# Kernel tuning notes

Measured on AMD Instinct MI355X. Metric: run time of the kernel, lower is better.

The kernel has to match this reference:

```python
import jax, jax.numpy as jnp
import numpy as np

# Dimensions: N batch, C chromosomes, GPC genes per chromosome, H hidden, S signature
N, C, GPC, H, S = 4096, 25, 80, 8, 32
G = C * GPC  # total genes (= input feature count D)
NB_CAT = 3   # each gene column is categorical in {0,1,2}
BN_EPS = 1e-5


def setup_inputs() -> dict:
    key = jax.random.key(0)
    k0, k1, k2, k3, k4 = jax.random.split(key, 5)
    # categorical gene columns
    x = jax.random.randint(k0, (N, G), 0, NB_CAT)
    # one embedding table per gene (genes_emb_sharing=False): (G, 3, H)
    emb_tables = jax.random.normal(k1, (G, NB_CAT, H), dtype=jnp.float32)
    # block-structured chromosome composition matrix (C, G): contiguous gene ranges
    cm = np.zeros((C, G), dtype=np.float32)
    for c in range(C):
        cm[c, c * GPC:(c + 1) * GPC] = 1.0
    chrom_mask = jnp.asarray(cm)
    # attention parameters (init: standard normal, as in the torch module)
    gene_att = jax.random.normal(k2, (C, H), dtype=jnp.float32)
    chrom_att = jax.random.normal(k3, (H,), dtype=jnp.float32)
    # final linear layer H -> S
    W = jax.random.normal(k4, (H, S), dtype=jnp.float32) / np.sqrt(H).astype(np.float32)
    b = jnp.zeros((S,), dtype=jnp.float32)
    return {"x": x, "emb_tables": emb_tables, "chrom_mask": chrom_mask,
            "gene_att": gene_att, "chrom_att": chrom_att, "W": W, "b": b}


def reference(x, emb_tables, chrom_mask, gene_att, chrom_att, W, b):
    G_ = emb_tables.shape[0]
    # entity embedding: per-gene table lookup -> (N, G, H)
    h = emb_tables[jnp.arange(G_)[None, :], x]

    # --- GeneAttentionLayer ---
    # fused form of einsum('ij,njk->nijk') -> transpose -> einsum('ij,kijm->kim'):
    # att[n,c,g] = chrom_mask[c,g] * <gene_att[c], h[n,g]>   (N, C, G)
    att = jnp.einsum('ch,ngh->ncg', gene_att, h) * chrom_mask[None]
    m = jax.lax.stop_gradient((att != 0).astype(att.dtype))  # detached byte mask
    att = jnp.exp(jax.nn.leaky_relu(att)) * m                # slope 0.01 matches torch
    att = att / att.sum(axis=2, keepdims=True)               # group softmax over genes
    chrom_emb = jnp.einsum('ncg,ngh->nch', att, h)           # (N, C, H)
    chrom_emb = jax.nn.relu(chrom_emb)

    # --- ChromAttentionLayer ---
    a = jnp.einsum('h,nch->nc', chrom_att, chrom_emb)        # (N, C)
    a = jnp.exp(jax.nn.leaky_relu(a))
    a = a / a.sum(axis=1, keepdims=True)
    sig = jnp.einsum('nc,nch->nh', a, chrom_emb)             # (N, H)
    sig = jax.nn.relu(sig)

    # linear + BatchNorm1d (training mode, gamma=1, beta=0, biased var)
    out = sig @ W + b
    mu = out.mean(axis=0)
    var = out.var(axis=0)
    return (out - mu) / jnp.sqrt(var + BN_EPS)
```

## Files before the change

### kernel.cpp

```cpp
#include <hip/hip_runtime.h>
#include <hip/hip_bf16.h>

#define NN   4096
#define CC   25
#define GPCg 80
#define HH   8
#define SS   32
#define GG   2000
#define TROWS 6000
#define SMB  16
#define NBLK (NN/SMB)
#define NQ   128
#define NTASK (SMB*CC)

#define CSTRIDE 241
#define A16_BYTES  96512
#define ATT_BYTES  12064
#define CE_BYTES   12800
#define SMEM_BYTES (A16_BYTES + ATT_BYTES + CE_BYTES)

typedef _Float16 h8 __attribute__((ext_vector_type(8)));

#define WS_RAW  0
#define WS_PART 131072

template<int CTRL>
__device__ __forceinline__ float dpp_add(float x) {
    int y = __builtin_amdgcn_mov_dpp(__float_as_int(x), CTRL, 0xF, 0xF, true);
    return x + __int_as_float(y);
}
__device__ __forceinline__ float red4(float x) {
    x = dpp_add<0xB1>(x);
    x = dpp_add<0x4E>(x);
    return x;
}

__global__ __launch_bounds__(512, 1) void k_fused(
    const int*   __restrict__ x, const float* __restrict__ emb,
    const float* __restrict__ gene_att, const float* __restrict__ chrom_att,
    const float* __restrict__ W, const float* __restrict__ b,
    float* __restrict__ raw, float2* __restrict__ part)
{
    extern __shared__ __align__(16) char smem[];
    _Float16* A16s  = (_Float16*)smem;
    _Float16* Att16 = (_Float16*)(smem + A16_BYTES);
    float*    ce    = (float*)(smem + A16_BYTES + ATT_BYTES);

    const int bid = blockIdx.x;
    const int n0  = bid * SMB;
    const int tid = threadIdx.x;
    const int qid = tid >> 2;
    const int q   = tid & 3;

    auto prefetch = [&](int r, int* dst) {
        const int task = r * NQ + qid;
        if (task < NTASK) {
            const int sm = task / CC;
            const int c  = task - sm * CC;
            const int* xp = x + (size_t)(n0 + sm) * GG + c * GPCg + q;
            #pragma unroll
            for (int j = 0; j < 20; ++j) dst[j] = xp[4 * j];
        }
    };

    auto compute = [&](int r, const int* xv) {
        const int task = r * NQ + qid;
        if (task < NTASK) {
            const int sm = task / CC;
            const int c  = task - sm * CC;
            const int base = c * CSTRIDE + 3 * q;

            h8 acc0, acc1;
            #pragma unroll
            for (int h = 0; h < HH; ++h) { acc0[h] = (_Float16)0.f; acc1[h] = (_Float16)0.f; }
            float asum = 0.f;

            #pragma unroll
            for (int j = 0; j < 20; ++j) {
                const int p = base + j * 12 + xv[j];
                h8 a = *(const h8*)(A16s + (size_t)p * HH);
                if (j & 1) acc1 += a; else acc0 += a;
                asum += (float)Att16[p];
            }

            float f0 = (float)acc0[0] + (float)acc1[0];
            float f1 = (float)acc0[1] + (float)acc1[1];
            float f2 = (float)acc0[2] + (float)acc1[2];
            float f3 = (float)acc0[3] + (float)acc1[3];
            float f4 = (float)acc0[4] + (float)acc1[4];
            float f5 = (float)acc0[5] + (float)acc1[5];
            float f6 = (float)acc0[6] + (float)acc1[6];
            float f7 = (float)acc0[7] + (float)acc1[7];
            f0 = red4(f0); f1 = red4(f1); f2 = red4(f2); f3 = red4(f3);
            f4 = red4(f4); f5 = red4(f5); f6 = red4(f6); f7 = red4(f7);
            asum = red4(asum);

            const float s = 1.f / asum;
            float va = f0, vb = f1;
            if (q == 1) { va = f2; vb = f3; }
            if (q == 2) { va = f4; vb = f5; }
            if (q == 3) { va = f6; vb = f7; }
            va = fmaxf(va * s, 0.f);
            vb = fmaxf(vb * s, 0.f);
            *(float2*)(ce + sm * (CC*HH) + c * HH + 2 * q) = make_float2(va, vb);
        }
    };

    int bufA[20], bufB[20];

    prefetch(0, bufA);

    for (int l = tid; l < TROWS; l += 512) {
        const int g    = l / 3;
        const int xv   = l - g * 3;
        const int c    = g / GPCg;
        const int gloc = g - c * GPCg;
        const int p    = c * CSTRIDE + gloc * 3 + xv;

        const float4* ep = (const float4*)(emb + (size_t)l * HH);
        float4 e0 = ep[0], e1 = ep[1];
        float ev[HH] = {e0.x, e0.y, e0.z, e0.w, e1.x, e1.y, e1.z, e1.w};
        float logit = 0.f;
        #pragma unroll
        for (int h = 0; h < HH; ++h) logit += gene_att[c * HH + h] * ev[h];
        float att = 0.f;
        if (logit != 0.f) {
            float lr = (logit >= 0.f) ? logit : 0.01f * logit;
            att = expf(lr);
        }
        h8 rr;
        #pragma unroll
        for (int h = 0; h < HH; ++h) rr[h] = (_Float16)(att * ev[h] * 0.00390625f);
        *(h8*)(A16s + (size_t)p * HH) = rr;
        Att16[p] = (_Float16)(att * 0.00390625f);
    }
    __syncthreads();

    prefetch(1, bufB); compute(0, bufA);
    prefetch(2, bufA); compute(1, bufB);
    prefetch(3, bufB); compute(2, bufA);
    compute(3, bufB);
    __syncthreads();

    const int half = tid >> 5;
    const int j    = tid & 31;
    const int n    = n0 + half;

    float cev[HH];
    float a = 0.f;
    if (j < CC) {
        const float4* p4 = (const float4*)(ce + half * (CC*HH) + j * HH);
        float4 v0 = p4[0], v1 = p4[1];
        cev[0]=v0.x; cev[1]=v0.y; cev[2]=v0.z; cev[3]=v0.w;
        cev[4]=v1.x; cev[5]=v1.y; cev[6]=v1.z; cev[7]=v1.w;
        float d = 0.f;
        #pragma unroll
        for (int h = 0; h < HH; ++h) d += chrom_att[h] * cev[h];
        float lr = (d >= 0.f) ? d : 0.01f * d;
        a = expf(lr);
    } else {
        #pragma unroll
        for (int h = 0; h < HH; ++h) cev[h] = 0.f;
    }

    float asum2 = a;
    #pragma unroll
    for (int off = 16; off >= 1; off >>= 1) asum2 += __shfl_xor(asum2, off, 32);
    const float an = a / asum2;

    float sig[HH];
    #pragma unroll
    for (int h = 0; h < HH; ++h) sig[h] = an * cev[h];
    #pragma unroll
    for (int off = 16; off >= 1; off >>= 1) {
        #pragma unroll
        for (int h = 0; h < HH; ++h) sig[h] += __shfl_xor(sig[h], off, 32);
    }
    #pragma unroll
    for (int h = 0; h < HH; ++h) sig[h] = fmaxf(sig[h], 0.f);

    float o = b[j];
    #pragma unroll
    for (int h = 0; h < HH; ++h) o += sig[h] * W[h * SS + j];
    raw[(size_t)n * SS + j] = o;

    float* psum = (float*)smem;
    float* psq  = psum + SMB * SS;
    psum[half * SS + j] = o;
    psq [half * SS + j] = o * o;
    __syncthreads();
    if (tid < SS) {
        float s1 = 0.f, s2 = 0.f;
        #pragma unroll
        for (int r = 0; r < SMB; ++r) { s1 += psum[r * SS + tid]; s2 += psq[r * SS + tid]; }
        part[(size_t)bid * SS + tid] = make_float2(s1, s2);
    }
}

__global__ __launch_bounds__(256) void k_bn(
    const float2* __restrict__ part, const float* __restrict__ raw,
    float* __restrict__ out)
{
    __shared__ float a1[8][SS], a2[8][SS];
    __shared__ float2 ms[SS];

    const int tid   = threadIdx.x;
    const int col   = tid & 31;
    const int chunk = tid >> 5;

    float s1 = 0.f, s2 = 0.f;
    for (int i = chunk * 32; i < chunk * 32 + 32; ++i) {
        float2 p = part[(size_t)i * SS + col];
        s1 += p.x; s2 += p.y;
    }
    a1[chunk][col] = s1; a2[chunk][col] = s2;
    __syncthreads();
    if (tid < SS) {
        float t1 = 0.f, t2 = 0.f;
        #pragma unroll
        for (int r = 0; r < 8; ++r) { t1 += a1[r][tid]; t2 += a2[r][tid]; }
        float mu  = t1 / (float)NN;
        float var = t2 / (float)NN - mu * mu;
        ms[tid] = make_float2(mu, rsqrtf(var + 1e-5f));
    }
    __syncthreads();

    const int n_loc = tid >> 3;
    const int s4    = tid & 7;
    const size_t off = ((size_t)(blockIdx.x * 32 + n_loc) * SS) + s4 * 4;
    float4 v = *(const float4*)(raw + off);
    float4 o;
    o.x = (v.x - ms[s4*4+0].x) * ms[s4*4+0].y;
    o.y = (v.y - ms[s4*4+1].x) * ms[s4*4+1].y;
    o.z = (v.z - ms[s4*4+2].x) * ms[s4*4+2].y;
    o.w = (v.w - ms[s4*4+3].x) * ms[s4*4+3].y;
    *(float4*)(out + off) = o;
}

extern "C" void kernel_launch(void* const* d_in, const int* in_sizes, int n_in,
                              void* d_out, int out_size, void* d_ws, size_t ws_size,
                              hipStream_t stream) {
    const int*   x         = (const int*)  d_in[0];
    const float* emb       = (const float*)d_in[1];
    const float* gene_att  = (const float*)d_in[3];
    const float* chrom_att = (const float*)d_in[4];
    const float* W         = (const float*)d_in[5];
    const float* b         = (const float*)d_in[6];
    float* out = (float*)d_out;

    float*  fws  = (float*)d_ws;
    float*  raw  = fws + WS_RAW;
    float2* part = (float2*)(fws + WS_PART);

    (void)hipFuncSetAttribute((const void*)k_fused,
                              hipFuncAttributeMaxDynamicSharedMemorySize,
                              (int)SMEM_BYTES);

    k_fused<<<NBLK, 512, SMEM_BYTES, stream>>>(x, emb, gene_att, chrom_att, W, b, raw, part);
    k_bn   <<<NN/32, 256, 0, stream>>>(part, raw, out);
}
```

Baseline: 22.01 us.

## Use 1024-thread blocks with two lanes per task and upfront x loads

The fused kernel now launches 1024 threads per block. Each (sample, chromosome) task is handled by a pair of lanes covering 40 genes each, instead of four lanes over four software-pipelined rounds. All categorical indices are loaded into registers before the table-build phase, so the global loads overlap with the shared-memory table construction and no longer need prefetch rounds. This costs more registers per thread (40 indices) and a larger block, leaving 400 of the 512 lane pairs doing work.

Measured after the change: 33.16 us. +50.6%, slower.

```diff
diff --git a/kernel.cpp b/kernel.cpp
--- a/kernel.cpp
+++ b/kernel.cpp
@@ -10,7 +10,8 @@
 #define TROWS 6000
 #define SMB  16
 #define NBLK (NN/SMB)
-#define NQ   128
+#define NTH  1024
+#define NPAIR (NTH/2)
 #define NTASK (SMB*CC)
 
 #define CSTRIDE 241
@@ -29,13 +30,11 @@
     int y = __builtin_amdgcn_mov_dpp(__float_as_int(x), CTRL, 0xF, 0xF, true);
     return x + __int_as_float(y);
 }
-__device__ __forceinline__ float red4(float x) {
-    x = dpp_add<0xB1>(x);
-    x = dpp_add<0x4E>(x);
-    return x;
-}
-
-__global__ __launch_bounds__(512, 1) void k_fused(
+__device__ __forceinline__ float red2(float x) {
+    return dpp_add<0xB1>(x);
+}
+
+__global__ __launch_bounds__(NTH, 1) void k_fused(
     const int*   __restrict__ x, const float* __restrict__ emb,
     const float* __restrict__ gene_att, const float* __restrict__ chrom_att,
     const float* __restrict__ W, const float* __restrict__ b,
@@ -49,80 +48,33 @@
     const int bid = blockIdx.x;
     const int n0  = bid * SMB;
     const int tid = threadIdx.x;
-    const int qid = tid >> 2;
-    const int q   = tid & 3;
-
-    auto prefetch = [&](int r, int* dst) {
-        const int task = r * NQ + qid;
-        if (task < NTASK) {
-            const int sm = task / CC;
-            const int c  = task - sm * CC;
-            const int* xp = x + (size_t)(n0 + sm) * GG + c * GPCg + q;
-            #pragma unroll
-            for (int j = 0; j < 20; ++j) dst[j] = xp[4 * j];
-        }
-    };
-
-    auto compute = [&](int r, const int* xv) {
-        const int task = r * NQ + qid;
-        if (task < NTASK) {
-            const int sm = task / CC;
-            const int c  = task - sm * CC;
-            const int base = c * CSTRIDE + 3 * q;
-
-            h8 acc0, acc1;
-            #pragma unroll
-            for (int h = 0; h < HH; ++h) { acc0[h] = (_Float16)0.f; acc1[h] = (_Float16)0.f; }
-            float asum = 0.f;
-
-            #pragma unroll
-            for (int j = 0; j < 20; ++j) {
-                const int p = base + j * 12 + xv[j];
-                h8 a = *(const h8*)(A16s + (size_t)p * HH);
-                if (j & 1) acc1 += a; else acc0 += a;
-                asum += (float)Att16[p];
-            }
-
-            float f0 = (float)acc0[0] + (float)acc1[0];
-            float f1 = (float)acc0[1] + (float)acc1[1];
-            float f2 = (float)acc0[2] + (float)acc1[2];
-            float f3 = (float)acc0[3] + (float)acc1[3];
-            float f4 = (float)acc0[4] + (float)acc1[4];
-            float f5 = (float)acc0[5] + (float)acc1[5];
-            float f6 = (float)acc0[6] + (float)acc1[6];
-            float f7 = (float)acc0[7] + (float)acc1[7];
-            f0 = red4(f0); f1 = red4(f1); f2 = red4(f2); f3 = red4(f3);
-            f4 = red4(f4); f5 = red4(f5); f6 = red4(f6); f7 = red4(f7);
-            asum = red4(asum);
-
-            const float s = 1.f / asum;
-            float va = f0, vb = f1;
-            if (q == 1) { va = f2; vb = f3; }
-            if (q == 2) { va = f4; vb = f5; }
-            if (q == 3) { va = f6; vb = f7; }
-            va = fmaxf(va * s, 0.f);
-            vb = fmaxf(vb * s, 0.f);
-            *(float2*)(ce + sm * (CC*HH) + c * HH + 2 * q) = make_float2(va, vb);
-        }
-    };
-
-    int bufA[20], bufB[20];
-
-    prefetch(0, bufA);
-
-    for (int l = tid; l < TROWS; l += 512) {
+    const int pid = tid >> 1;
+    const int q   = tid & 1;
+    const bool active = (pid < NTASK);
+
+    const int sm = pid / CC;
+    const int c  = active ? (pid - sm * CC) : 0;
+
+    int xv[40];
+    if (active) {
+        const int* xp = x + (size_t)(n0 + sm) * GG + c * GPCg + q;
+        #pragma unroll
+        for (int j = 0; j < 40; ++j) xv[j] = xp[2 * j];
+    }
+
+    for (int l = tid; l < TROWS; l += NTH) {
         const int g    = l / 3;
-        const int xv   = l - g * 3;
-        const int c    = g / GPCg;
-        const int gloc = g - c * GPCg;
-        const int p    = c * CSTRIDE + gloc * 3 + xv;
+        const int xc   = l - g * 3;
+        const int cc   = g / GPCg;
+        const int gloc = g - cc * GPCg;
+        const int p    = cc * CSTRIDE + gloc * 3 + xc;
 
         const float4* ep = (const float4*)(emb + (size_t)l * HH);
         float4 e0 = ep[0], e1 = ep[1];
         float ev[HH] = {e0.x, e0.y, e0.z, e0.w, e1.x, e1.y, e1.z, e1.w};
         float logit = 0.f;
         #pragma unroll
-        for (int h = 0; h < HH; ++h) logit += gene_att[c * HH + h] * ev[h];
+        for (int h = 0; h < HH; ++h) logit += gene_att[cc * HH + h] * ev[h];
         float att = 0.f;
         if (logit != 0.f) {
             float lr = (logit >= 0.f) ? logit : 0.01f * logit;
@@ -136,60 +88,101 @@
     }
     __syncthreads();
 
-    prefetch(1, bufB); compute(0, bufA);
-    prefetch(2, bufA); compute(1, bufB);
-    prefetch(3, bufB); compute(2, bufA);
-    compute(3, bufB);
+    if (active) {
+        const int base = c * CSTRIDE + 3 * q;
+
+        h8 acc0, acc1;
+        #pragma unroll
+        for (int h = 0; h < HH; ++h) { acc0[h] = (_Float16)0.f; acc1[h] = (_Float16)0.f; }
+        float asum = 0.f;
+
+        #pragma unroll
+        for (int j = 0; j < 40; ++j) {
+            const int p = base + 6 * j + xv[j];
+            h8 a = *(const h8*)(A16s + (size_t)p * HH);
+            if (j & 1) acc1 += a; else acc0 += a;
+            asum += (float)Att16[p];
+        }
+
+        float f0 = (float)acc0[0] + (float)acc1[0];
+        float f1 = (float)acc0[1] + (float)acc1[1];
+        float f2 = (float)acc0[2] + (float)acc1[2];
+        float f3 = (float)acc0[3] + (float)acc1[3];
+        float f4 = (float)acc0[4] + (float)acc1[4];
+        float f5 = (float)acc0[5] + (float)acc1[5];
+        float f6 = (float)acc0[6] + (float)acc1[6];
+        float f7 = (float)acc0[7] + (float)acc1[7];
+        f0 = red2(f0); f1 = red2(f1); f2 = red2(f2); f3 = red2(f3);
+        f4 = red2(f4); f5 = red2(f5); f6 = red2(f6); f7 = red2(f7);
+        asum = red2(asum);
+
+        const float s = 1.f / asum;
+        float4 o;
+        if (q == 0) {
+            o = make_float4(f0, f1, f2, f3);
+        } else {
+            o = make_float4(f4, f5, f6, f7);
+        }
+        o.x = fmaxf(o.x * s, 0.f);
+        o.y = fmaxf(o.y * s, 0.f);
+        o.z = fmaxf(o.z * s, 0.f);
+        o.w = fmaxf(o.w * s, 0.f);
+        *(float4*)(ce + sm * (CC*HH) + c * HH + 4 * q) = o;
+    }
     __syncthreads();
 
     const int half = tid >> 5;
     const int j    = tid & 31;
-    const int n    = n0 + half;
-
-    float cev[HH];
-    float a = 0.f;
-    if (j < CC) {
-        const float4* p4 = (const float4*)(ce + half * (CC*HH) + j * HH);
-        float4 v0 = p4[0], v1 = p4[1];
-        cev[0]=v0.x; cev[1]=v0.y; cev[2]=v0.z; cev[3]=v0.w;
-        cev[4]=v1.x; cev[5]=v1.y; cev[6]=v1.z; cev[7]=v1.w;
-        float d = 0.f;
-        #pragma unroll
-        for (int h = 0; h < HH; ++h) d += chrom_att[h] * cev[h];
-        float lr = (d >= 0.f) ? d : 0.01f * d;
-        a = expf(lr);
-    } else {
-        #pragma unroll
-        for (int h = 0; h < HH; ++h) cev[h] = 0.f;
-    }
-
-    float asum2 = a;
-    #pragma unroll
-    for (int off = 16; off >= 1; off >>= 1) asum2 += __shfl_xor(asum2, off, 32);
-    const float an = a / asum2;
-
-    float sig[HH];
-    #pragma unroll
-    for (int h = 0; h < HH; ++h) sig[h] = an * cev[h];
-    #pragma unroll
-    for (int off = 16; off >= 1; off >>= 1) {
-        #pragma unroll
-        for (int h = 0; h < HH; ++h) sig[h] += __shfl_xor(sig[h], off, 32);
-    }
-    #pragma unroll
-    for (int h = 0; h < HH; ++h) sig[h] = fmaxf(sig[h], 0.f);
-
-    float o = b[j];
-    #pragma unroll
-    for (int h = 0; h < HH; ++h) o += sig[h] * W[h * SS + j];
-    raw[(size_t)n * SS + j] = o;
-
-    float* psum = (float*)smem;
-    float* psq  = psum + SMB * SS;
-    psum[half * SS + j] = o;
-    psq [half * SS + j] = o * o;
+    if (half < SMB) {
+        const int n = n0 + half;
+
+        float cev[HH];
+        float a = 0.f;
+        if (j < CC) {
+            const float4* p4 = (const float4*)(ce + half * (CC*HH) + j * HH);
+            float4 v0 = p4[0], v1 = p4[1];
+            cev[0]=v0.x; cev[1]=v0.y; cev[2]=v0.z; cev[3]=v0.w;
+            cev[4]=v1.x; cev[5]=v1.y; cev[6]=v1.z; cev[7]=v1.w;
+            float d = 0.f;
+            #pragma unroll
+            for (int h = 0; h < HH; ++h) d += chrom_att[h] * cev[h];
+            float lr = (d >= 0.f) ? d : 0.01f * d;
+            a = expf(lr);
+        } else {
+            #pragma unroll
+            for (int h = 0; h < HH; ++h) cev[h] = 0.f;
+        }
+
+        float asum2 = a;
+        #pragma unroll
+        for (int off = 16; off >= 1; off >>= 1) asum2 += __shfl_xor(asum2, off, 32);
+        const float an = a / asum2;
+
+        float sig[HH];
+        #pragma unroll
+        for (int h = 0; h < HH; ++h) sig[h] = an * cev[h];
+        #pragma unroll
+        for (int off = 16; off >= 1; off >>= 1) {
+            #pragma unroll
+            for (int h = 0; h < HH; ++h) sig[h] += __shfl_xor(sig[h], off, 32);
+        }
+        #pragma unroll
+        for (int h = 0; h < HH; ++h) sig[h] = fmaxf(sig[h], 0.f);
+
+        float o = b[j];
+        #pragma unroll
+        for (int h = 0; h < HH; ++h) o += sig[h] * W[h * SS + j];
+        raw[(size_t)n * SS + j] = o;
+
+        float* psum = (float*)smem;
+        float* psq  = psum + SMB * SS;
+        psum[half * SS + j] = o;
+        psq [half * SS + j] = o * o;
+    }
     __syncthreads();
     if (tid < SS) {
+        const float* psum = (const float*)smem;
+        const float* psq  = psum + SMB * SS;
         float s1 = 0.f, s2 = 0.f;
         #pragma unroll
         for (int r = 0; r < SMB; ++r) { s1 += psum[r * SS + tid]; s2 += psq[r * SS + tid]; }
@@ -256,6 +249,6 @@
                               hipFuncAttributeMaxDynamicSharedMemorySize,
                               (int)SMEM_BYTES);
 
-    k_fused<<<NBLK, 512, SMEM_BYTES, stream>>>(x, emb, gene_att, chrom_att, W, b, raw, part);
+    k_fused<<<NBLK, NTH, SMEM_BYTES, stream>>>(x, emb, gene_att, chrom_att, W, b, raw, part);
     k_bn   <<<NN/32, 256, 0, stream>>>(part, raw, out);
 }
```

## Use 768 threads and contiguous int4 index loads per gene quarter

Applied to the files above, without the earlier changes.

Raises the fused kernel block size from 512 to 768 threads, so the 400 chromosome tasks per block finish in three rounds instead of four. Each quarter-thread now owns 20 contiguous genes and loads their indices as int4 vectors instead of strided scalar loads, and the attention-sum accumulator is split in two. The epilogue is guarded so that only the first 16 groups of 32 threads take part. The larger block raises register pressure under the launch bound, and the unchanged table-build loop now leaves some threads idle in its last pass.

Result: faster. 20.15 us (-8.5%).

```diff
diff --git a/kernel.cpp b/kernel.cpp
--- a/kernel.cpp
+++ b/kernel.cpp
@@ -10,8 +10,10 @@
 #define TROWS 6000
 #define SMB  16
 #define NBLK (NN/SMB)
-#define NQ   128
+#define NTH  768
+#define NQ   (NTH/4)
 #define NTASK (SMB*CC)
+#define NROUND 3
 
 #define CSTRIDE 241
 #define A16_BYTES  96512
@@ -35,7 +37,7 @@
     return x;
 }
 
-__global__ __launch_bounds__(512, 1) void k_fused(
+__global__ __launch_bounds__(NTH, 1) void k_fused(
     const int*   __restrict__ x, const float* __restrict__ emb,
     const float* __restrict__ gene_att, const float* __restrict__ chrom_att,
     const float* __restrict__ W, const float* __restrict__ b,
@@ -57,9 +59,12 @@
         if (task < NTASK) {
             const int sm = task / CC;
             const int c  = task - sm * CC;
-            const int* xp = x + (size_t)(n0 + sm) * GG + c * GPCg + q;
-            #pragma unroll
-            for (int j = 0; j < 20; ++j) dst[j] = xp[4 * j];
+            const int4* xp = (const int4*)(x + (size_t)(n0 + sm) * GG + c * GPCg + q * 20);
+            #pragma unroll
+            for (int i = 0; i < 5; ++i) {
+                int4 v = xp[i];
+                dst[4*i+0] = v.x; dst[4*i+1] = v.y; dst[4*i+2] = v.z; dst[4*i+3] = v.w;
+            }
         }
     };
 
@@ -68,19 +73,19 @@
         if (task < NTASK) {
             const int sm = task / CC;
             const int c  = task - sm * CC;
-            const int base = c * CSTRIDE + 3 * q;
+            const int base = c * CSTRIDE + 3 * (q * 20);
 
             h8 acc0, acc1;
             #pragma unroll
             for (int h = 0; h < HH; ++h) { acc0[h] = (_Float16)0.f; acc1[h] = (_Float16)0.f; }
-            float asum = 0.f;
+            float asum0 = 0.f, asum1 = 0.f;
 
             #pragma unroll
             for (int j = 0; j < 20; ++j) {
-                const int p = base + j * 12 + xv[j];
+                const int p = base + 3 * j + xv[j];
                 h8 a = *(const h8*)(A16s + (size_t)p * HH);
-                if (j & 1) acc1 += a; else acc0 += a;
-                asum += (float)Att16[p];
+                if (j & 1) { acc1 += a; asum1 += (float)Att16[p]; }
+                else       { acc0 += a; asum0 += (float)Att16[p]; }
             }
 
             float f0 = (float)acc0[0] + (float)acc1[0];
@@ -93,7 +98,7 @@
             float f7 = (float)acc0[7] + (float)acc1[7];
             f0 = red4(f0); f1 = red4(f1); f2 = red4(f2); f3 = red4(f3);
             f4 = red4(f4); f5 = red4(f5); f6 = red4(f6); f7 = red4(f7);
-            asum = red4(asum);
+            float asum = red4(asum0 + asum1);
 
             const float s = 1.f / asum;
             float va = f0, vb = f1;
@@ -110,19 +115,19 @@
 
     prefetch(0, bufA);
 
-    for (int l = tid; l < TROWS; l += 512) {
+    for (int l = tid; l < TROWS; l += NTH) {
         const int g    = l / 3;
-        const int xv   = l - g * 3;
-        const int c    = g / GPCg;
-        const int gloc = g - c * GPCg;
-        const int p    = c * CSTRIDE + gloc * 3 + xv;
+        const int xc   = l - g * 3;
+        const int cc   = g / GPCg;
+        const int gloc = g - cc * GPCg;
+        const int p    = cc * CSTRIDE + gloc * 3 + xc;
 
         const float4* ep = (const float4*)(emb + (size_t)l * HH);
         float4 e0 = ep[0], e1 = ep[1];
         float ev[HH] = {e0.x, e0.y, e0.z, e0.w, e1.x, e1.y, e1.z, e1.w};
         float logit = 0.f;
         #pragma unroll
-        for (int h = 0; h < HH; ++h) logit += gene_att[c * HH + h] * ev[h];
+        for (int h = 0; h < HH; ++h) logit += gene_att[cc * HH + h] * ev[h];
         float att = 0.f;
         if (logit != 0.f) {
             float lr = (logit >= 0.f) ? logit : 0.01f * logit;
@@ -138,58 +143,61 @@
 
     prefetch(1, bufB); compute(0, bufA);
     prefetch(2, bufA); compute(1, bufB);
-    prefetch(3, bufB); compute(2, bufA);
-    compute(3, bufB);
+    compute(2, bufA);
     __syncthreads();
 
     const int half = tid >> 5;
     const int j    = tid & 31;
-    const int n    = n0 + half;
-
-    float cev[HH];
-    float a = 0.f;
-    if (j < CC) {
-        const float4* p4 = (const float4*)(ce + half * (CC*HH) + j * HH);
-        float4 v0 = p4[0], v1 = p4[1];
-        cev[0]=v0.x; cev[1]=v0.y; cev[2]=v0.z; cev[3]=v0.w;
-        cev[4]=v1.x; cev[5]=v1.y; cev[6]=v1.z; cev[7]=v1.w;
-        float d = 0.f;
-        #pragma unroll
-        for (int h = 0; h < HH; ++h) d += chrom_att[h] * cev[h];
-        float lr = (d >= 0.f) ? d : 0.01f * d;
-        a = expf(lr);
-    } else {
-        #pragma unroll
-        for (int h = 0; h < HH; ++h) cev[h] = 0.f;
-    }
-
-    float asum2 = a;
-    #pragma unroll
-    for (int off = 16; off >= 1; off >>= 1) asum2 += __shfl_xor(asum2, off, 32);
-    const float an = a / asum2;
-
-    float sig[HH];
-    #pragma unroll
-    for (int h = 0; h < HH; ++h) sig[h] = an * cev[h];
-    #pragma unroll
-    for (int off = 16; off >= 1; off >>= 1) {
-        #pragma unroll
-        for (int h = 0; h < HH; ++h) sig[h] += __shfl_xor(sig[h], off, 32);
-    }
-    #pragma unroll
-    for (int h = 0; h < HH; ++h) sig[h] = fmaxf(sig[h], 0.f);
-
-    float o = b[j];
-    #pragma unroll
-    for (int h = 0; h < HH; ++h) o += sig[h] * W[h * SS + j];
-    raw[(size_t)n * SS + j] = o;
-
-    float* psum = (float*)smem;
-    float* psq  = psum + SMB * SS;
-    psum[half * SS + j] = o;
-    psq [half * SS + j] = o * o;
+    if (half < SMB) {
+        const int n = n0 + half;
+
+        float cev[HH];
+        float a = 0.f;
+        if (j < CC) {
+            const float4* p4 = (const float4*)(ce + half * (CC*HH) + j * HH);
+            float4 v0 = p4[0], v1 = p4[1];
+            cev[0]=v0.x; cev[1]=v0.y; cev[2]=v0.z; cev[3]=v0.w;
+            cev[4]=v1.x; cev[5]=v1.y; cev[6]=v1.z; cev[7]=v1.w;
+            float d = 0.f;
+            #pragma unroll
+            for (int h = 0; h < HH; ++h) d += chrom_att[h] * cev[h];
+            float lr = (d >= 0.f) ? d : 0.01f * d;
+            a = expf(lr);
+        } else {
+            #pragma unroll
+            for (int h = 0; h < HH; ++h) cev[h] = 0.f;
+        }
+
+        float asum2 = a;
+        #pragma unroll
+        for (int off = 16; off >= 1; off >>= 1) asum2 += __shfl_xor(asum2, off, 32);
+        const float an = a / asum2;
+
+        float sig[HH];
+        #pragma unroll
+        for (int h = 0; h < HH; ++h) sig[h] = an * cev[h];
+        #pragma unroll
+        for (int off = 16; off >= 1; off >>= 1) {
+            #pragma unroll
+            for (int h = 0; h < HH; ++h) sig[h] += __shfl_xor(sig[h], off, 32);
+        }
+        #pragma unroll
+        for (int h = 0; h < HH; ++h) sig[h] = fmaxf(sig[h], 0.f);
+
+        float o = b[j];
+        #pragma unroll
+        for (int h = 0; h < HH; ++h) o += sig[h] * W[h * SS + j];
+        raw[(size_t)n * SS + j] = o;
+
+        float* psum = (float*)smem;
+        float* psq  = psum + SMB * SS;
+        psum[half * SS + j] = o;
+        psq [half * SS + j] = o * o;
+    }
     __syncthreads();
     if (tid < SS) {
+        const float* psum = (const float*)smem;
+        const float* psq  = psum + SMB * SS;
         float s1 = 0.f, s2 = 0.f;
         #pragma unroll
         for (int r = 0; r < SMB; ++r) { s1 += psum[r * SS + tid]; s2 += psq[r * SS + tid]; }
@@ -256,6 +264,6 @@
                               hipFuncAttributeMaxDynamicSharedMemorySize,
                               (int)SMEM_BYTES);
 
-    k_fused<<<NBLK, 512, SMEM_BYTES, stream>>>(x, emb, gene_att, chrom_att, W, b, raw, part);
+    k_fused<<<NBLK, NTH, SMEM_BYTES, stream>>>(x, emb, gene_att, chrom_att, W, b, raw, part);
     k_bn   <<<NN/32, 256, 0, stream>>>(part, raw, out);
 }
```
